# Kernel optimization log

Hardware: AMD Instinct MI355X
Metric: run time of the kernel (lower is better)

Reference implementation:

```python
import jax, jax.numpy as jnp
import numpy as np

# dims: M scalars (0e), K vectors (1e) in input; T = tp_features; N = batch of atoms
M, K, T, N = 128, 64, 64, 131072
D_IN = M + 3 * K  # 320, e3nn layout: [128x0e | 64x1e flattened as (mul, 3)]


def _act_norm(f):
    # e3nn Activation normalizes act so E_{z~N(0,1)}[act(z)^2] = 1
    z = np.linspace(-8.0, 8.0, 20001)
    pdf = np.exp(-0.5 * z * z) / np.sqrt(2.0 * np.pi)
    return float(np.sqrt(np.trapz(f(z) ** 2 * pdf, z)))

C_SILU = _act_norm(lambda z: z / (1.0 + np.exp(-z)))
C_RELU = _act_norm(lambda z: np.maximum(z, 0.0))
INV_SQRT_M = float(1.0 / np.sqrt(M))
INV_SQRT_K = float(1.0 / np.sqrt(K))
INV_SQRT_3 = float(1.0 / np.sqrt(3.0))  # wigner_3j(1,1,0) = delta_ij/sqrt(3)
TP_NORM = float(1.0 / np.sqrt(2.0 * T * T))  # fan-in over the 2 paths into 0e


def setup_inputs() -> dict:
    key = jax.random.key(0)
    ks = jax.random.split(key, 11)
    f32 = jnp.float32
    return {
        "x": jax.random.normal(ks[0], (N, D_IN), f32),
        "input_shift": jnp.zeros((D_IN,), f32),
        "output_scale": jnp.ones((), f32),
        # PerceptronLayer 1: Linear (Mx0e+Kx1e) -> ((M+K)x0e + Kx1e)
        "w0_1": jax.random.normal(ks[1], (M, M + K), f32),
        "b0_1": jnp.zeros((M + K,), f32),
        "w1_1": jax.random.normal(ks[2], (K, K), f32),
        # PerceptronLayer 2 (same irreps, resnet applies)
        "w0_2": jax.random.normal(ks[3], (M, M + K), f32),
        "b0_2": jnp.zeros((M + K,), f32),
        "w1_2": jax.random.normal(ks[4], (K, K), f32),
        # linear_out: (Mx0e+Kx1e) -> (Tx0e+Tx1e)
        "w0_o": jax.random.normal(ks[5], (M, T), f32),
        "b0_o": jnp.zeros((T,), f32),
        "w1_o": jax.random.normal(ks[6], (K, T), f32),
        # FullyConnectedTensorProduct (tp, tp) -> 1x0e: paths 0e*0e->0e, 1e*1e->0e
        "w_tp0": jax.random.normal(ks[7], (T, T), f32),
        "w_tp1": jax.random.normal(ks[8], (T, T), f32),
    }


def _linear(xs, xv, w0, b0, w1):
    # e3nn o3.Linear: per-irrep dense mixing with 1/sqrt(fan_in), bias on 0e only
    ys = xs @ w0 * INV_SQRT_M + b0          # [N, M+K] scalars + gates
    yv = jnp.einsum('nki,kj->nji', xv, w1) * INV_SQRT_K  # [N, K, 3]
    return ys, yv


def _gate(ys, yv):
    # e3nn Gate: silu on 0e scalars, relu on 0e gates, gate the 1e vectors
    s = jax.nn.silu(ys[:, :M]) / C_SILU     # [N, M]
    g = jax.nn.relu(ys[:, M:]) / C_RELU     # [N, K]
    return s, yv * g[:, :, None]


def reference(x, input_shift, output_scale,
              w0_1, b0_1, w1_1, w0_2, b0_2, w1_2,
              w0_o, b0_o, w1_o, w_tp0, w_tp1):
    x = x - input_shift
    xs = x[:, :M]                           # [N, M] 0e block
    xv = x[:, M:].reshape(-1, K, 3)         # [N, K, 3] 1e block
    for (w0, b0, w1) in ((w0_1, b0_1, w1_1), (w0_2, b0_2, w1_2)):
        ys, yv = _linear(xs, xv, w0, b0, w1)
        s, v = _gate(ys, yv)
        xs = xs + s                         # resnet: irreps_in == irreps_out
        xv = xv + v
    # linear_out -> irreps_tp = Tx0e + Tx1e
    zs = xs @ w0_o * INV_SQRT_M + b0_o                    # [N, T]
    zv = jnp.einsum('nki,kj->nji', xv, w1_o) * INV_SQRT_K # [N, T, 3]
    # FullyConnectedTensorProduct(z, z) -> 0e (avoid [N,T,T] blowup)
    y0 = jnp.sum((zs @ w_tp0) * zs, axis=-1)                                    # [N]
    y1 = jnp.sum(jnp.einsum('nui,uv->nvi', zv, w_tp1) * zv, axis=(1, 2)) * INV_SQRT_3
    y = (y0 + y1) * TP_NORM / output_scale
    return y[:, None]
```

## Files before the change

### kernel.cpp

```cpp
#include <hip/hip_runtime.h>
#include <math.h>


typedef _Float16 f16;
typedef _Float16 f16x8 __attribute__((ext_vector_type(8)));
typedef __fp16   fp16x2 __attribute__((ext_vector_type(2)));
typedef float    f32x4 __attribute__((ext_vector_type(4)));
typedef int      i32x4 __attribute__((ext_vector_type(4)));

#define MFMA16(a, b, c) __builtin_amdgcn_mfma_f32_16x16x32_f16(a, b, c, 0, 0, 0)

constexpr float INV_SQRT_M = 0.08838834764831845f;
constexpr float INV_SQRT_K = 0.125f;
constexpr float INV_SQRT_3 = 0.57735026918962576f;
constexpr float TP_NORM    = 0.011048543456039806f;

#define OFF_W01 0
#define OFF_W11 24576
#define OFF_W02 28672
#define OFF_W12 53248
#define OFF_W0O 57344
#define OFF_W1O 65536
#define OFF_TP0 69632
#define OFF_TP1 73728
#define PACK_UNITS 9728
#define FB01 38912
#define FB02 39104
#define FB0O 39296
#define TOTAL_UNITS (PACK_UNITS + 448)

#define LDS_W1     24576
#define LDS_BIAS_F 14336
#define LDS_W0O    0
#define LDS_W1O    8192
#define LDS_TP0    12288
#define LDS_TP1    16384
#define LDS_B0O_F  10240

#define NTHR 512

__global__ void init_consts_kernel(float* __restrict__ ws) {
    __shared__ double red[1024];
    const int t = threadIdx.x;
    double acc_s = 0.0, acc_r = 0.0;
    for (int i = t; i <= 20000; i += 1024) {
        const double z = -8.0 + (16.0 * (double)i) / 20000.0;
        const double pdf = exp(-0.5 * z * z) / 2.5066282746310002;
        const double sil = z / (1.0 + exp(-z));
        const double wgt = (i == 0 || i == 20000) ? 0.5 : 1.0;
        acc_s += wgt * sil * sil * pdf;
        if (z > 0.0) acc_r += wgt * z * z * pdf;
    }
    red[t] = acc_s;
    __syncthreads();
    for (int o = 512; o > 0; o >>= 1) { if (t < o) red[t] += red[t + o]; __syncthreads(); }
    const double tot_s = red[0];
    __syncthreads();
    red[t] = acc_r;
    __syncthreads();
    for (int o = 512; o > 0; o >>= 1) { if (t < o) red[t] += red[t + o]; __syncthreads(); }
    if (t == 0) {
        const double dz = 16.0 / 20000.0;
        ws[0] = (float)(1.0 / sqrt(tot_s * dz));
        ws[1] = (float)(1.0 / sqrt(red[0] * dz));
    }
}

__global__ void pack_weights(const float* __restrict__ w01, const float* __restrict__ w11,
                             const float* __restrict__ w02, const float* __restrict__ w12,
                             const float* __restrict__ w0o, const float* __restrict__ w1o,
                             const float* __restrict__ tp0, const float* __restrict__ tp1,
                             const float* __restrict__ b01, const float* __restrict__ b02,
                             const float* __restrict__ b0o,
                             f16* __restrict__ dst) {
    int u = blockIdx.x * 256 + threadIdx.x;
    if (u >= TOTAL_UNITS) return;
    if (u >= PACK_UNITS) {
        const int idx = u - PACK_UNITS;
        float* dstF = (float*)dst;
        if (idx < 192)      dstF[FB01 + idx] = b01[idx];
        else if (idx < 384) dstF[FB02 + (idx - 192)] = b02[idx - 192];
        else                dstF[FB0O + (idx - 384)] = b0o[idx - 384];
        return;
    }
    const float* src; int NC, base, lu = u; float sc;
    if      (lu < 3072) {            src = w01; NC = 192; base = OFF_W01; sc = INV_SQRT_M; }
    else if (lu < 3584) { lu -= 3072; src = w11; NC = 64;  base = OFF_W11; sc = INV_SQRT_K; }
    else if (lu < 6656) { lu -= 3584; src = w02; NC = 192; base = OFF_W02; sc = INV_SQRT_M; }
    else if (lu < 7168) { lu -= 6656; src = w12; NC = 64;  base = OFF_W12; sc = INV_SQRT_K; }
    else if (lu < 8192) { lu -= 7168; src = w0o; NC = 64;  base = OFF_W0O; sc = INV_SQRT_M; }
    else if (lu < 8704) { lu -= 8192; src = w1o; NC = 64;  base = OFF_W1O; sc = INV_SQRT_K; }
    else if (lu < 9216) { lu -= 8704; src = tp0; NC = 64;  base = OFF_TP0; sc = 1.0f; }
    else                { lu -= 9216; src = tp1; NC = 64;  base = OFF_TP1; sc = INV_SQRT_3; }
    const int lane = lu & 63;
    const int frag = lu >> 6;
    const int NT = NC >> 4;
    const int kstep = frag / NT, nj = frag - kstep * NT;
    const int gl  = lane >> 4;
    const int col = nj * 16 + (lane & 15);
    f16 tmp[8];
    #pragma unroll
    for (int e = 0; e < 8; ++e) {
        const int row = kstep * 32 + ((e >> 2) << 4) + (gl << 2) + (e & 3);
        tmp[e] = (f16)(src[(size_t)row * NC + col] * sc);
    }
    *(f16x8*)&dst[(size_t)(base) + (size_t)lu * 8] = *(f16x8*)tmp;
}

__device__ __forceinline__ int pk2i(float a, float b) {
    union { fp16x2 h; int i; } u;
    u.h = __builtin_amdgcn_cvt_pkrtz(a, b);
    return u.i;
}

__device__ __forceinline__ f16x8 packB(f32x4 t0, f32x4 t1) {
    union { i32x4 i; f16x8 v; } u;
    u.i[0] = pk2i(t0[0], t0[1]);
    u.i[1] = pk2i(t0[2], t0[3]);
    u.i[2] = pk2i(t1[0], t1[1]);
    u.i[3] = pk2i(t1[2], t1[3]);
    return u.v;
}

union Frag { f16x8 v; fp16x2 h2[4]; };

__device__ __forceinline__ void resblock32(
    Frag (&xsS)[2][4], Frag (&xvS)[2][3][2],
    const f16* lds, float invCS, float invCR, int l, int g)
{
    const float* biasF = (const float*)lds + LDS_BIAS_F;

    f16x8 xsB[2][4];
    #pragma unroll
    for (int h = 0; h < 2; ++h)
        #pragma unroll
        for (int ks = 0; ks < 4; ++ks)
            xsB[h][ks] = xsS[h][ks].v;

    float gate[2][4][4];
    #pragma unroll
    for (int nj = 0; nj < 12; ++nj) {
        f32x4 acc0 = {0.f, 0.f, 0.f, 0.f}, acc1 = {0.f, 0.f, 0.f, 0.f};
        #pragma unroll
        for (int ks = 0; ks < 4; ++ks) {
            const f16x8 a = *(const f16x8*)&lds[(size_t)((ks * 12 + nj) * 64 + l) * 8];
            acc0 = MFMA16(a, xsB[0][ks], acc0);
            acc1 = MFMA16(a, xsB[1][ks], acc1);
        }
        const f32x4 bias = *(const f32x4*)&biasF[nj * 16 + g * 4];
        #pragma unroll
        for (int h = 0; h < 2; ++h) {
            const f32x4 acc = h ? acc1 : acc0;
            if (nj < 8) {
                float s[4];
                #pragma unroll
                for (int r = 0; r < 4; ++r) {
                    const float ys = acc[r] + bias[r];
                    s[r] = ys * __builtin_amdgcn_rcpf(1.0f + __expf(-ys)) * invCS;
                }
                xsS[h][nj >> 1].h2[2 * (nj & 1)]     += __builtin_amdgcn_cvt_pkrtz(s[0], s[1]);
                xsS[h][nj >> 1].h2[2 * (nj & 1) + 1] += __builtin_amdgcn_cvt_pkrtz(s[2], s[3]);
            } else {
                #pragma unroll
                for (int r = 0; r < 4; ++r) {
                    const float ys = acc[r] + bias[r];
                    gate[h][nj - 8][r] = fmaxf(ys, 0.f) * invCR;
                }
            }
        }
    }

    f16x8 xvB[2][3][2];
    #pragma unroll
    for (int h = 0; h < 2; ++h)
        #pragma unroll
        for (int i = 0; i < 3; ++i)
            #pragma unroll
            for (int ks = 0; ks < 2; ++ks)
                xvB[h][i][ks] = xvS[h][i][ks].v;

    #pragma unroll
    for (int i = 0; i < 3; ++i)
        #pragma unroll
        for (int nj = 0; nj < 4; ++nj) {
            f32x4 acc0 = {0.f, 0.f, 0.f, 0.f}, acc1 = {0.f, 0.f, 0.f, 0.f};
            #pragma unroll
            for (int ks = 0; ks < 2; ++ks) {
                const f16x8 a = *(const f16x8*)&lds[LDS_W1 + (size_t)((ks * 4 + nj) * 64 + l) * 8];
                acc0 = MFMA16(a, xvB[0][i][ks], acc0);
                acc1 = MFMA16(a, xvB[1][i][ks], acc1);
            }
            #pragma unroll
            for (int h = 0; h < 2; ++h) {
                const f32x4 acc = h ? acc1 : acc0;
                float u[4];
                #pragma unroll
                for (int r = 0; r < 4; ++r)
                    u[r] = acc[r] * gate[h][nj][r];
                xvS[h][i][nj >> 1].h2[2 * (nj & 1)]     += __builtin_amdgcn_cvt_pkrtz(u[0], u[1]);
                xvS[h][i][nj >> 1].h2[2 * (nj & 1) + 1] += __builtin_amdgcn_cvt_pkrtz(u[2], u[3]);
            }
        }
}

__global__ __launch_bounds__(NTHR, 2)
void corrnet_lds(const float* __restrict__ x, const float* __restrict__ shift,
                 const float* __restrict__ oscale,
                 const f16* __restrict__ wp, const float* __restrict__ consts,
                 float* __restrict__ out)
{
    __shared__ __align__(16) f16 smem[29056];
    float* smemF = (float*)smem;
    const float* wpF = (const float*)wp;

    const int t = threadIdx.x;
    const int l = t & 63;
    const int w = __builtin_amdgcn_readfirstlane(t >> 6);
    const int g = l >> 4;
    const int c = l & 15;
    const size_t n0 = (size_t)blockIdx.x * 256 + (size_t)w * 32;

    const float invCS = consts[0], invCR = consts[1];
    const float inv_os = 1.0f / oscale[0];

    #pragma unroll
    for (int it = 0; it < 7; ++it) {
        const int u = it * NTHR + t;
        *(f16x8*)&smem[(size_t)u * 8] = *(const f16x8*)&wp[(size_t)u * 8];
    }
    if (t < 48)
        ((f32x4*)&smemF[LDS_BIAS_F])[t] = ((const f32x4*)&wpF[FB01])[t];

    Frag xsS[2][4];
    Frag xvS[2][3][2];
    #pragma unroll
    for (int h = 0; h < 2; ++h) {
        const float* xrow = x + (n0 + h * 16 + c) * 320;
        #pragma unroll
        for (int ks = 0; ks < 4; ++ks) {
            const int col = ks * 32 + g * 4;
            const f32x4 t0 = *(const f32x4*)(xrow + col)      - *(const f32x4*)(shift + col);
            const f32x4 t1 = *(const f32x4*)(xrow + col + 16) - *(const f32x4*)(shift + col + 16);
            xsS[h][ks].v = packB(t0, t1);
        }
        f32x4 tmp[3][4];
        #pragma unroll
        for (int tau = 0; tau < 4; ++tau) {
            const int col = 128 + 3 * (tau * 16 + g * 4);
            const f32x4 a0 = *(const f32x4*)(xrow + col)     - *(const f32x4*)(shift + col);
            const f32x4 a1 = *(const f32x4*)(xrow + col + 4) - *(const f32x4*)(shift + col + 4);
            const f32x4 a2 = *(const f32x4*)(xrow + col + 8) - *(const f32x4*)(shift + col + 8);
            float arr[12];
            #pragma unroll
            for (int e = 0; e < 4; ++e) {
                arr[e] = a0[e]; arr[4 + e] = a1[e]; arr[8 + e] = a2[e];
            }
            #pragma unroll
            for (int r = 0; r < 4; ++r)
                #pragma unroll
                for (int i = 0; i < 3; ++i)
                    tmp[i][tau][r] = arr[3 * r + i];
        }
        #pragma unroll
        for (int i = 0; i < 3; ++i)
            #pragma unroll
            for (int ks = 0; ks < 2; ++ks)
                xvS[h][i][ks].v = packB(tmp[i][2 * ks], tmp[i][2 * ks + 1]);
    }

    __syncthreads();
    resblock32(xsS, xvS, smem, invCS, invCR, l, g);
    __syncthreads();

    #pragma unroll
    for (int it = 0; it < 7; ++it) {
        const int u = it * NTHR + t;
        *(f16x8*)&smem[(size_t)u * 8] = *(const f16x8*)&wp[(size_t)(OFF_W02) + (size_t)u * 8];
    }
    if (t < 48)
        ((f32x4*)&smemF[LDS_BIAS_F])[t] = ((const f32x4*)&wpF[FB02])[t];
    __syncthreads();
    resblock32(xsS, xvS, smem, invCS, invCR, l, g);
    __syncthreads();

    #pragma unroll
    for (int it = 0; it < 5; ++it) {
        const int u = it * NTHR + t;
        *(f16x8*)&smem[(size_t)u * 8] = *(const f16x8*)&wp[(size_t)(OFF_W0O) + (size_t)u * 8];
    }
    if (t < 16)
        ((f32x4*)&smemF[LDS_B0O_F])[t] = ((const f32x4*)&wpF[FB0O])[t];
    __syncthreads();

    f32x4 zs[2][4];
    #pragma unroll
    for (int nj = 0; nj < 4; ++nj) {
        f32x4 acc0 = {0.f, 0.f, 0.f, 0.f}, acc1 = {0.f, 0.f, 0.f, 0.f};
        #pragma unroll
        for (int ks = 0; ks < 4; ++ks) {
            const f16x8 a = *(const f16x8*)&smem[LDS_W0O + (size_t)((ks * 4 + nj) * 64 + l) * 8];
            acc0 = MFMA16(a, xsS[0][ks].v, acc0);
            acc1 = MFMA16(a, xsS[1][ks].v, acc1);
        }
        const f32x4 bias = *(const f32x4*)&smemF[LDS_B0O_F + nj * 16 + g * 4];
        #pragma unroll
        for (int r = 0; r < 4; ++r) {
            zs[0][nj][r] = acc0[r] + bias[r];
            zs[1][nj][r] = acc1[r] + bias[r];
        }
    }

    float part[2]  = {0.f, 0.f};
    float part1[2] = {0.f, 0.f};

    {
        f16x8 zsB[2][2];
        #pragma unroll
        for (int h = 0; h < 2; ++h)
            #pragma unroll
            for (int ks = 0; ks < 2; ++ks)
                zsB[h][ks] = packB(zs[h][2 * ks], zs[h][2 * ks + 1]);
        #pragma unroll
        for (int nj = 0; nj < 4; ++nj) {
            f32x4 acc0 = {0.f, 0.f, 0.f, 0.f}, acc1 = {0.f, 0.f, 0.f, 0.f};
            #pragma unroll
            for (int ks = 0; ks < 2; ++ks) {
                const f16x8 a = *(const f16x8*)&smem[LDS_TP0 + (size_t)((ks * 4 + nj) * 64 + l) * 8];
                acc0 = MFMA16(a, zsB[0][ks], acc0);
                acc1 = MFMA16(a, zsB[1][ks], acc1);
            }
            #pragma unroll
            for (int r = 0; r < 4; ++r) {
                part[0] += acc0[r] * zs[0][nj][r];
                part[1] += acc1[r] * zs[1][nj][r];
            }
        }
    }

    #pragma unroll
    for (int i = 0; i < 3; ++i) {
        f32x4 zv[2][4];
        #pragma unroll
        for (int nj = 0; nj < 4; ++nj) {
            f32x4 acc0 = {0.f, 0.f, 0.f, 0.f}, acc1 = {0.f, 0.f, 0.f, 0.f};
            #pragma unroll
            for (int ks = 0; ks < 2; ++ks) {
                const f16x8 a = *(const f16x8*)&smem[LDS_W1O + (size_t)((ks * 4 + nj) * 64 + l) * 8];
                acc0 = MFMA16(a, xvS[0][i][ks].v, acc0);
                acc1 = MFMA16(a, xvS[1][i][ks].v, acc1);
            }
            #pragma unroll
            for (int r = 0; r < 4; ++r) {
                zv[0][nj][r] = acc0[r];
                zv[1][nj][r] = acc1[r];
            }
        }
        f16x8 zvB[2][2];
        #pragma unroll
        for (int h = 0; h < 2; ++h)
            #pragma unroll
            for (int ks = 0; ks < 2; ++ks)
                zvB[h][ks] = packB(zv[h][2 * ks], zv[h][2 * ks + 1]);
        #pragma unroll
        for (int nj = 0; nj < 4; ++nj) {
            f32x4 acc0 = {0.f, 0.f, 0.f, 0.f}, acc1 = {0.f, 0.f, 0.f, 0.f};
            #pragma unroll
            for (int ks = 0; ks < 2; ++ks) {
                const f16x8 a = *(const f16x8*)&smem[LDS_TP1 + (size_t)((ks * 4 + nj) * 64 + l) * 8];
                acc0 = MFMA16(a, zvB[0][ks], acc0);
                acc1 = MFMA16(a, zvB[1][ks], acc1);
            }
            #pragma unroll
            for (int r = 0; r < 4; ++r) {
                part1[0] += acc0[r] * zv[0][nj][r];
                part1[1] += acc1[r] * zv[1][nj][r];
            }
        }
    }
    #pragma unroll
    for (int h = 0; h < 2; ++h)
        part[h] += part1[h];

    #pragma unroll
    for (int h = 0; h < 2; ++h) {
        part[h] += __shfl_xor(part[h], 16, 64);
        part[h] += __shfl_xor(part[h], 32, 64);
    }

    if (l < 16)
        out[n0 + l] = part[0] * TP_NORM * inv_os;
    else if (l < 32)
        out[n0 + 16 + (l - 16)] = part[1] * TP_NORM * inv_os;
}

extern "C" void kernel_launch(void* const* d_in, const int* in_sizes, int n_in,
                              void* d_out, int out_size, void* d_ws, size_t ws_size,
                              hipStream_t stream) {
    const float* x      = (const float*)d_in[0];
    const float* shift  = (const float*)d_in[1];
    const float* oscale = (const float*)d_in[2];
    const float* w01    = (const float*)d_in[3];
    const float* b01    = (const float*)d_in[4];
    const float* w11    = (const float*)d_in[5];
    const float* w02    = (const float*)d_in[6];
    const float* b02    = (const float*)d_in[7];
    const float* w12    = (const float*)d_in[8];
    const float* w0o    = (const float*)d_in[9];
    const float* b0o    = (const float*)d_in[10];
    const float* w1o    = (const float*)d_in[11];
    const float* wtp0   = (const float*)d_in[12];
    const float* wtp1   = (const float*)d_in[13];
    float* out    = (float*)d_out;
    float* consts = (float*)d_ws;
    f16*   wp     = (f16*)((char*)d_ws + 16);

    init_consts_kernel<<<1, 1024, 0, stream>>>(consts);
    pack_weights<<<(TOTAL_UNITS + 255) / 256, 256, 0, stream>>>(
        w01, w11, w02, w12, w0o, w1o, wtp0, wtp1, b01, b02, b0o, wp);

    const int nblocks = 131072 / 256;
    corrnet_lds<<<nblocks, NTHR, 0, stream>>>(
        x, shift, oscale, wp, consts, out);
}
```

Baseline: 75.65 us.

## Merge setup kernels, software-prefetch scalar weights, batch vector MFMAs before gating

Folds the normalization-constant computation into the weight-packing kernel as an extra block, removing one launch. It also double-buffers the LDS weight and bias loads in the scalar linear loop so the next column's operands load while the current MFMAs run. The vector linear now issues all four MFMA column pairs before applying the gates, and drops the scalar wave-index readfirstlane. The changes raise register pressure under the existing launch bounds, and the 256-thread constants block now serially loops over more points.

```diff
diff --git a/kernel.cpp b/kernel.cpp
--- a/kernel.cpp
+++ b/kernel.cpp
@@ -39,40 +39,40 @@
 
 #define NTHR 512
 
-__global__ void init_consts_kernel(float* __restrict__ ws) {
-    __shared__ double red[1024];
-    const int t = threadIdx.x;
-    double acc_s = 0.0, acc_r = 0.0;
-    for (int i = t; i <= 20000; i += 1024) {
-        const double z = -8.0 + (16.0 * (double)i) / 20000.0;
-        const double pdf = exp(-0.5 * z * z) / 2.5066282746310002;
-        const double sil = z / (1.0 + exp(-z));
-        const double wgt = (i == 0 || i == 20000) ? 0.5 : 1.0;
-        acc_s += wgt * sil * sil * pdf;
-        if (z > 0.0) acc_r += wgt * z * z * pdf;
-    }
-    red[t] = acc_s;
-    __syncthreads();
-    for (int o = 512; o > 0; o >>= 1) { if (t < o) red[t] += red[t + o]; __syncthreads(); }
-    const double tot_s = red[0];
-    __syncthreads();
-    red[t] = acc_r;
-    __syncthreads();
-    for (int o = 512; o > 0; o >>= 1) { if (t < o) red[t] += red[t + o]; __syncthreads(); }
-    if (t == 0) {
-        const double dz = 16.0 / 20000.0;
-        ws[0] = (float)(1.0 / sqrt(tot_s * dz));
-        ws[1] = (float)(1.0 / sqrt(red[0] * dz));
-    }
-}
-
-__global__ void pack_weights(const float* __restrict__ w01, const float* __restrict__ w11,
-                             const float* __restrict__ w02, const float* __restrict__ w12,
-                             const float* __restrict__ w0o, const float* __restrict__ w1o,
-                             const float* __restrict__ tp0, const float* __restrict__ tp1,
-                             const float* __restrict__ b01, const float* __restrict__ b02,
-                             const float* __restrict__ b0o,
-                             f16* __restrict__ dst) {
+__global__ void pack_and_consts(const float* __restrict__ w01, const float* __restrict__ w11,
+                                const float* __restrict__ w02, const float* __restrict__ w12,
+                                const float* __restrict__ w0o, const float* __restrict__ w1o,
+                                const float* __restrict__ tp0, const float* __restrict__ tp1,
+                                const float* __restrict__ b01, const float* __restrict__ b02,
+                                const float* __restrict__ b0o,
+                                f16* __restrict__ dst, float* __restrict__ ws) {
+    if (blockIdx.x == 40) {
+        __shared__ double red[256];
+        const int t = threadIdx.x;
+        double acc_s = 0.0, acc_r = 0.0;
+        for (int i = t; i <= 20000; i += 256) {
+            const double z = -8.0 + (16.0 * (double)i) / 20000.0;
+            const double pdf = exp(-0.5 * z * z) / 2.5066282746310002;
+            const double sil = z / (1.0 + exp(-z));
+            const double wgt = (i == 0 || i == 20000) ? 0.5 : 1.0;
+            acc_s += wgt * sil * sil * pdf;
+            if (z > 0.0) acc_r += wgt * z * z * pdf;
+        }
+        red[t] = acc_s;
+        __syncthreads();
+        for (int o = 128; o > 0; o >>= 1) { if (t < o) red[t] += red[t + o]; __syncthreads(); }
+        const double tot_s = red[0];
+        __syncthreads();
+        red[t] = acc_r;
+        __syncthreads();
+        for (int o = 128; o > 0; o >>= 1) { if (t < o) red[t] += red[t + o]; __syncthreads(); }
+        if (t == 0) {
+            const double dz = 16.0 / 20000.0;
+            ws[0] = (float)(1.0 / sqrt(tot_s * dz));
+            ws[1] = (float)(1.0 / sqrt(red[0] * dz));
+        }
+        return;
+    }
     int u = blockIdx.x * 256 + threadIdx.x;
     if (u >= TOTAL_UNITS) return;
     if (u >= PACK_UNITS) {
@@ -137,17 +137,31 @@
         for (int ks = 0; ks < 4; ++ks)
             xsB[h][ks] = xsS[h][ks].v;
 
+    f16x8 aP[4];
+    #pragma unroll
+    for (int ks = 0; ks < 4; ++ks)
+        aP[ks] = *(const f16x8*)&lds[(size_t)(ks * 12 * 64 + l) * 8];
+    f32x4 biasP = *(const f32x4*)&biasF[g * 4];
+
     float gate[2][4][4];
     #pragma unroll
     for (int nj = 0; nj < 12; ++nj) {
+        f16x8 aC[4];
+        #pragma unroll
+        for (int ks = 0; ks < 4; ++ks) aC[ks] = aP[ks];
+        const f32x4 bias = biasP;
+        if (nj < 11) {
+            #pragma unroll
+            for (int ks = 0; ks < 4; ++ks)
+                aP[ks] = *(const f16x8*)&lds[(size_t)((ks * 12 + nj + 1) * 64 + l) * 8];
+            biasP = *(const f32x4*)&biasF[(nj + 1) * 16 + g * 4];
+        }
         f32x4 acc0 = {0.f, 0.f, 0.f, 0.f}, acc1 = {0.f, 0.f, 0.f, 0.f};
         #pragma unroll
         for (int ks = 0; ks < 4; ++ks) {
-            const f16x8 a = *(const f16x8*)&lds[(size_t)((ks * 12 + nj) * 64 + l) * 8];
-            acc0 = MFMA16(a, xsB[0][ks], acc0);
-            acc1 = MFMA16(a, xsB[1][ks], acc1);
-        }
-        const f32x4 bias = *(const f32x4*)&biasF[nj * 16 + g * 4];
+            acc0 = MFMA16(aC[ks], xsB[0][ks], acc0);
+            acc1 = MFMA16(aC[ks], xsB[1][ks], acc1);
+        }
         #pragma unroll
         for (int h = 0; h < 2; ++h) {
             const f32x4 acc = h ? acc1 : acc0;
@@ -170,37 +184,33 @@
         }
     }
 
-    f16x8 xvB[2][3][2];
-    #pragma unroll
-    for (int h = 0; h < 2; ++h)
-        #pragma unroll
-        for (int i = 0; i < 3; ++i)
-            #pragma unroll
-            for (int ks = 0; ks < 2; ++ks)
-                xvB[h][i][ks] = xvS[h][i][ks].v;
-
-    #pragma unroll
-    for (int i = 0; i < 3; ++i)
+    #pragma unroll
+    for (int i = 0; i < 3; ++i) {
+        f32x4 av[2][4];
         #pragma unroll
         for (int nj = 0; nj < 4; ++nj) {
-            f32x4 acc0 = {0.f, 0.f, 0.f, 0.f}, acc1 = {0.f, 0.f, 0.f, 0.f};
+            f32x4 a0 = {0.f, 0.f, 0.f, 0.f}, a1 = {0.f, 0.f, 0.f, 0.f};
             #pragma unroll
             for (int ks = 0; ks < 2; ++ks) {
                 const f16x8 a = *(const f16x8*)&lds[LDS_W1 + (size_t)((ks * 4 + nj) * 64 + l) * 8];
-                acc0 = MFMA16(a, xvB[0][i][ks], acc0);
-                acc1 = MFMA16(a, xvB[1][i][ks], acc1);
-            }
+                a0 = MFMA16(a, xvS[0][i][ks].v, a0);
+                a1 = MFMA16(a, xvS[1][i][ks].v, a1);
+            }
+            av[0][nj] = a0;
+            av[1][nj] = a1;
+        }
+        #pragma unroll
+        for (int nj = 0; nj < 4; ++nj)
             #pragma unroll
             for (int h = 0; h < 2; ++h) {
-                const f32x4 acc = h ? acc1 : acc0;
                 float u[4];
                 #pragma unroll
                 for (int r = 0; r < 4; ++r)
-                    u[r] = acc[r] * gate[h][nj][r];
+                    u[r] = av[h][nj][r] * gate[h][nj][r];
                 xvS[h][i][nj >> 1].h2[2 * (nj & 1)]     += __builtin_amdgcn_cvt_pkrtz(u[0], u[1]);
                 xvS[h][i][nj >> 1].h2[2 * (nj & 1) + 1] += __builtin_amdgcn_cvt_pkrtz(u[2], u[3]);
             }
-        }
+    }
 }
 
 __global__ __launch_bounds__(NTHR, 2)
@@ -215,10 +225,9 @@
 
     const int t = threadIdx.x;
     const int l = t & 63;
-    const int w = __builtin_amdgcn_readfirstlane(t >> 6);
     const int g = l >> 4;
     const int c = l & 15;
-    const size_t n0 = (size_t)blockIdx.x * 256 + (size_t)w * 32;
+    const size_t n0 = (size_t)blockIdx.x * 256 + (size_t)(t >> 6) * 32;
 
     const float invCS = consts[0], invCR = consts[1];
     const float inv_os = 1.0f / oscale[0];
@@ -414,9 +423,8 @@
     float* consts = (float*)d_ws;
     f16*   wp     = (f16*)((char*)d_ws + 16);
 
-    init_consts_kernel<<<1, 1024, 0, stream>>>(consts);
-    pack_weights<<<(TOTAL_UNITS + 255) / 256, 256, 0, stream>>>(
-        w01, w11, w02, w12, w0o, w1o, wtp0, wtp1, b01, b02, b0o, wp);
+    pack_and_consts<<<41, 256, 0, stream>>>(
+        w01, w11, w02, w12, w0o, w1o, wtp0, wtp1, b01, b02, b0o, wp, consts);
 
     const int nblocks = 131072 / 256;
     corrnet_lds<<<nblocks, NTHR, 0, stream>>>(
```

Result: slower. 80.15 us (+5.9%).
